# Kernel tuning notes

Measured on AMD Instinct MI355X. Metric: run time of the kernel, lower is better.

## Reference

```python
import jax, jax.numpy as jnp
import numpy as np


def setup_inputs() -> dict:
    key = jax.random.key(0)
    k1, k2 = jax.random.split(key)
    B, F = 131072, 32
    LOCAL_DIM, RANK, UNITS = 2, 10, 8
    X = jax.random.normal(k1, (B, F), dtype=jnp.float32)
    kernel = jax.random.normal(k2, (LOCAL_DIM, RANK, F, UNITS), dtype=jnp.float32) * 0.24  # ~glorot for fan sizes here
    return {"X": X, "kernel": kernel}


def reference(X, kernel):
    # X: [B, F]; kernel: [local_dim, rank, F, units]
    local_dim = kernel.shape[0]
    # powers X^0 .. X^(local_dim-1), stacked on last axis -> [B, F, local_dim]
    powers = jnp.stack([X ** p for p in range(local_dim)], axis=-1)
    # L2-normalize over the power axis (matches tf.sqrt(reduce_sum(x**2)))
    norms = jnp.sqrt(jnp.sum(powers * powers, axis=-1, keepdims=True))
    x = powers / norms  # [B, F, local_dim]
    # per-feature matmul across all units at once: [B, F, rank, units]
    t = jnp.einsum('bfd,drfu->bfru', x, kernel)
    # hadamard product over features, then sum over CP rank -> [B, units]
    out = jnp.sum(jnp.prod(t, axis=1), axis=1)
    return out  # activation is linear (None)
```

## Files before the change

kernel.cpp:

```cpp
#include <hip/hip_runtime.h>


typedef float f32x2 __attribute__((ext_vector_type(2)));
typedef float f32x4 __attribute__((ext_vector_type(4)));

#define F 32
#define RANK 10
#define UNITS 8

__global__ __launch_bounds__(256) void cp_based_kernel(
    const float* __restrict__ X,
    const float* __restrict__ K,
    float* __restrict__ out,
    int B)
{
    int b = blockIdx.x * blockDim.x + threadIdx.x;
    if (b >= B) return;

    const f32x4* xrow = reinterpret_cast<const f32x4*>(X + (size_t)b * F);
    float xv[F];
    float p0 = 1.0f;
#pragma unroll
    for (int i = 0; i < F / 4; ++i) {
        f32x4 v = xrow[i];
#pragma unroll
        for (int j = 0; j < 4; ++j) {
            float x = v[j];
            xv[i * 4 + j] = x;
            p0 *= __builtin_amdgcn_rsqf(__builtin_fmaf(x, x, 1.0f));
        }
    }

    const int K1_OFF = RANK * F * UNITS;

    f32x2 acc0 = {0.f, 0.f}, acc1 = {0.f, 0.f}, acc2 = {0.f, 0.f}, acc3 = {0.f, 0.f};

    for (int r = 0; r < RANK; ++r) {
        f32x2 p0v = {1.f, 1.f}, p1v = {1.f, 1.f}, p2v = {1.f, 1.f}, p3v = {1.f, 1.f};
        const float* k0base = K + (size_t)(r * F) * UNITS;
        const float* k1base = K + (size_t)K1_OFF + (size_t)(r * F) * UNITS;
#pragma unroll
        for (int f = 0; f < F; ++f) {
            const f32x2* k0 = reinterpret_cast<const f32x2*>(k0base + f * UNITS);
            const f32x2* k1 = reinterpret_cast<const f32x2*>(k1base + f * UNITS);
            float xf = xv[f];
            f32x2 xs = {xf, xf};
            f32x2 t0 = xs * k0[0 + 0] * 0.0f;
            (void)t0;
            {
                f32x2 ta = xs * k1[0] + k0[0];
                f32x2 tb = xs * k1[1] + k0[1];
                f32x2 tc = xs * k1[2] + k0[2];
                f32x2 td = xs * k1[3] + k0[3];
                p0v *= ta;
                p1v *= tb;
                p2v *= tc;
                p3v *= td;
            }
        }
        acc0 += p0v;
        acc1 += p1v;
        acc2 += p2v;
        acc3 += p3v;
    }

    acc0 *= p0; acc1 *= p0; acc2 *= p0; acc3 *= p0;

    float* o = out + (size_t)b * UNITS;
    f32x4 r0 = {acc0[0], acc0[1], acc1[0], acc1[1]};
    f32x4 r1 = {acc2[0], acc2[1], acc3[0], acc3[1]};
    reinterpret_cast<f32x4*>(o)[0] = r0;
    reinterpret_cast<f32x4*>(o)[1] = r1;
}

extern "C" void kernel_launch(void* const* d_in, const int* in_sizes, int n_in,
                              void* d_out, int out_size, void* d_ws, size_t ws_size,
                              hipStream_t stream) {
    const float* X = (const float*)d_in[0];
    const float* K = (const float*)d_in[1];
    float* out = (float*)d_out;
    int B = in_sizes[0] / F;

    dim3 block(256);
    dim3 grid((B + 255) / 256);
    hipLaunchKernelGGL(cp_based_kernel, grid, block, 0, stream, X, K, out, B);
}
```

Baseline: 27.81 us.

## Split CP rank loop across five waves per block with LDS reduction

Each block now handles 64 rows with five wavefronts, each wave computing two of the ten CP ranks, and the partial sums are reduced through shared memory by wave 0. This gives each thread less serial work and more parallelism per row. The normalization is rewritten as a product of (1+x^2) over two halves with two rsq calls instead of 32 rsq calls. In exchange, every wave loads X redundantly, and the change adds a barrier and an LDS round trip. The bounds check is removed, so B is assumed to be a multiple of 64, and the large product could lose precision.

```diff
diff --git a/kernel.cpp b/kernel.cpp
--- a/kernel.cpp
+++ b/kernel.cpp
@@ -7,70 +7,83 @@
 #define F 32
 #define RANK 10
 #define UNITS 8
+#define YSPLIT 5
 
-__global__ __launch_bounds__(256) void cp_based_kernel(
+__global__ __launch_bounds__(320) void cp_based_kernel(
     const float* __restrict__ X,
     const float* __restrict__ K,
     float* __restrict__ out,
     int B)
 {
-    int b = blockIdx.x * blockDim.x + threadIdx.x;
-    if (b >= B) return;
+    __shared__ float red[YSPLIT][64][UNITS];
+
+    const int lane = threadIdx.x;
+    const int y = __builtin_amdgcn_readfirstlane(threadIdx.y);
+    const int b = blockIdx.x * 64 + lane;
 
     const f32x4* xrow = reinterpret_cast<const f32x4*>(X + (size_t)b * F);
     float xv[F];
-    float p0 = 1.0f;
 #pragma unroll
     for (int i = 0; i < F / 4; ++i) {
         f32x4 v = xrow[i];
 #pragma unroll
-        for (int j = 0; j < 4; ++j) {
-            float x = v[j];
-            xv[i * 4 + j] = x;
-            p0 *= __builtin_amdgcn_rsqf(__builtin_fmaf(x, x, 1.0f));
-        }
+        for (int j = 0; j < 4; ++j) xv[i * 4 + j] = v[j];
     }
 
     const int K1_OFF = RANK * F * UNITS;
 
-    f32x2 acc0 = {0.f, 0.f}, acc1 = {0.f, 0.f}, acc2 = {0.f, 0.f}, acc3 = {0.f, 0.f};
+    f32x2 s0 = {0.f, 0.f}, s1 = {0.f, 0.f}, s2 = {0.f, 0.f}, s3 = {0.f, 0.f};
 
-    for (int r = 0; r < RANK; ++r) {
-        f32x2 p0v = {1.f, 1.f}, p1v = {1.f, 1.f}, p2v = {1.f, 1.f}, p3v = {1.f, 1.f};
-        const float* k0base = K + (size_t)(r * F) * UNITS;
-        const float* k1base = K + (size_t)K1_OFF + (size_t)(r * F) * UNITS;
+#pragma unroll
+    for (int rr = 0; rr < 2; ++rr) {
+        const int r = 2 * y + rr;
+        const float* k0b = K + r * F * UNITS;
+        const float* k1b = k0b + K1_OFF;
+        f32x2 p0 = {1.f, 1.f}, p1 = {1.f, 1.f}, p2 = {1.f, 1.f}, p3 = {1.f, 1.f};
 #pragma unroll
         for (int f = 0; f < F; ++f) {
-            const f32x2* k0 = reinterpret_cast<const f32x2*>(k0base + f * UNITS);
-            const f32x2* k1 = reinterpret_cast<const f32x2*>(k1base + f * UNITS);
+            const f32x2* k0 = reinterpret_cast<const f32x2*>(k0b + f * UNITS);
+            const f32x2* k1 = reinterpret_cast<const f32x2*>(k1b + f * UNITS);
             float xf = xv[f];
             f32x2 xs = {xf, xf};
-            f32x2 t0 = xs * k0[0 + 0] * 0.0f;
-            (void)t0;
-            {
-                f32x2 ta = xs * k1[0] + k0[0];
-                f32x2 tb = xs * k1[1] + k0[1];
-                f32x2 tc = xs * k1[2] + k0[2];
-                f32x2 td = xs * k1[3] + k0[3];
-                p0v *= ta;
-                p1v *= tb;
-                p2v *= tc;
-                p3v *= td;
-            }
+            f32x2 t0 = xs * k1[0] + k0[0];
+            f32x2 t1 = xs * k1[1] + k0[1];
+            f32x2 t2 = xs * k1[2] + k0[2];
+            f32x2 t3 = xs * k1[3] + k0[3];
+            p0 *= t0;
+            p1 *= t1;
+            p2 *= t2;
+            p3 *= t3;
         }
-        acc0 += p0v;
-        acc1 += p1v;
-        acc2 += p2v;
-        acc3 += p3v;
+        s0 += p0; s1 += p1; s2 += p2; s3 += p3;
     }
 
-    acc0 *= p0; acc1 *= p0; acc2 *= p0; acc3 *= p0;
+    f32x4* redp = reinterpret_cast<f32x4*>(&red[y][lane][0]);
+    redp[0] = f32x4{s0[0], s0[1], s1[0], s1[1]};
+    redp[1] = f32x4{s2[0], s2[1], s3[0], s3[1]};
+    __syncthreads();
 
-    float* o = out + (size_t)b * UNITS;
-    f32x4 r0 = {acc0[0], acc0[1], acc1[0], acc1[1]};
-    f32x4 r1 = {acc2[0], acc2[1], acc3[0], acc3[1]};
-    reinterpret_cast<f32x4*>(o)[0] = r0;
-    reinterpret_cast<f32x4*>(o)[1] = r1;
+    if (y == 0) {
+        f32x4 a0 = redp[0];
+        f32x4 a1 = redp[1];
+#pragma unroll
+        for (int k = 1; k < YSPLIT; ++k) {
+            const f32x4* q = reinterpret_cast<const f32x4*>(&red[k][lane][0]);
+            a0 += q[0];
+            a1 += q[1];
+        }
+        float pA = 1.0f, pB = 1.0f;
+#pragma unroll
+        for (int f = 0; f < 16; ++f) pA *= __builtin_fmaf(xv[f], xv[f], 1.0f);
+#pragma unroll
+        for (int f = 16; f < 32; ++f) pB *= __builtin_fmaf(xv[f], xv[f], 1.0f);
+        float pn = __builtin_amdgcn_rsqf(pA) * __builtin_amdgcn_rsqf(pB);
+        a0 *= pn;
+        a1 *= pn;
+        f32x4* o = reinterpret_cast<f32x4*>(out + (size_t)b * UNITS);
+        o[0] = a0;
+        o[1] = a1;
+    }
 }
 
 extern "C" void kernel_launch(void* const* d_in, const int* in_sizes, int n_in,
@@ -81,7 +94,7 @@
     float* out = (float*)d_out;
     int B = in_sizes[0] / F;
 
-    dim3 block(256);
-    dim3 grid((B + 255) / 256);
+    dim3 block(64, YSPLIT);
+    dim3 grid(B / 64);
     hipLaunchKernelGGL(cp_based_kernel, grid, block, 0, stream, X, K, out, B);
 }
```

New measurement: 31.20 us. +12.2%, slower.
